# Kernel tuning notes

Hardware: AMD Instinct MI355X
Metric: run time of the kernel (lower is better)

Reference implementation:

```python
import jax, jax.numpy as jnp
import numpy as np

N_NODES = 50000
N_EDGES = 800000
C_IN = 64
HID = 3
C_OUT = 128
ATTR = 6


def setup_inputs() -> dict:
    key = jax.random.key(0)
    ks = jax.random.split(key, 16)
    inp = {
        "x": jax.random.normal(ks[0], (N_NODES, C_IN), dtype=jnp.float32),
        "edge_index0": jax.random.randint(ks[1], (2, N_EDGES), 0, N_NODES, dtype=jnp.int32).astype(jnp.int64),
        "edge_attr0": jax.random.normal(ks[2], (N_EDGES, ATTR), dtype=jnp.float32),
        "edge_index1": jax.random.randint(ks[3], (2, N_EDGES), 0, N_NODES, dtype=jnp.int32).astype(jnp.int64),
        "edge_attr1": jax.random.normal(ks[4], (N_EDGES, ATTR), dtype=jnp.float32),
        "W_in0": jax.random.normal(ks[5], (ATTR, HID * C_IN), dtype=jnp.float32) * 0.1,
        "b_in0": jax.random.normal(ks[6], (HID * C_IN,), dtype=jnp.float32) * 0.1,
        "W_out0": jax.random.normal(ks[7], (HID * C_IN, C_OUT), dtype=jnp.float32) * 0.05,
        "b_out0": jax.random.normal(ks[8], (C_OUT,), dtype=jnp.float32) * 0.05,
        "W_in1": jax.random.normal(ks[9], (ATTR, HID * C_IN), dtype=jnp.float32) * 0.1,
        "b_in1": jax.random.normal(ks[10], (HID * C_IN,), dtype=jnp.float32) * 0.1,
        "W_out1": jax.random.normal(ks[11], (HID * C_IN, C_OUT), dtype=jnp.float32) * 0.05,
        "b_out1": jax.random.normal(ks[12], (C_OUT,), dtype=jnp.float32) * 0.05,
    }
    return inp


def _spatial_graph_conv(x, edge_index, edge_attr, W_in, b_in, W_out, b_out):
    # PyG MessagePassing default flow: x_j = x[edge_index[0]] (source),
    # aggregate (add) at edge_index[1] (target).
    src, dst = edge_index[0], edge_index[1]
    n_nodes, c_in = x.shape
    x_j = x[src]                                   # [E, C]
    scaling = jax.nn.relu(edge_attr @ W_in + b_in)  # [E, 3C]
    n_edges = x_j.shape[0]
    msg = (scaling.reshape(n_edges, c_in, -1) * x_j[:, :, None]).reshape(n_edges, -1)  # [E, 3C]
    aggr = jax.ops.segment_sum(msg, dst, num_segments=n_nodes)  # [N, 3C]
    return jnp.tanh(aggr @ W_out + b_out)  # [N, C_OUT]; dropout p=0 -> identity


def reference(x, edge_index0, edge_attr0, edge_index1, edge_attr1,
              W_in0, b_in0, W_out0, b_out0, W_in1, b_in1, W_out1, b_out1):
    # aGCN_conv with use_A=2: two independent SpatialGraphConv layers, concat on feature dim.
    y0 = _spatial_graph_conv(x, edge_index0, edge_attr0, W_in0, b_in0, W_out0, b_out0)
    y1 = _spatial_graph_conv(x, edge_index1, edge_attr1, W_in1, b_in1, W_out1, b_out1)
    return jnp.concatenate([y0, y1], axis=1)  # [N, 2*C_OUT]
```

## Files before the change

kernel.cpp:

```cpp
#include <hip/hip_runtime.h>

#define N_NODES 50000
#define N_EDGES 800000
#define C_IN 64
#define HID 3
#define C_OUTC 128
#define ATTR 6
#define K3 192
#define NREAL 1563
#define NBK2 1564
#define CAP2 768
#define EPB2 2048
#define P1B2 391
#define AGS 200
#define SORTCAP (CAP2 + 96)

typedef _Float16 half8  __attribute__((ext_vector_type(8)));
typedef float    floatx4 __attribute__((ext_vector_type(4)));

#define RFL(x) __builtin_amdgcn_readfirstlane((int)(x))

static __device__ __forceinline__ float lo16f(unsigned v) {
    unsigned short s = (unsigned short)(v & 0xFFFF);
    _Float16 h;
    __builtin_memcpy(&h, &s, 2);
    return (float)h;
}
static __device__ __forceinline__ float hi16f(unsigned v) { return lo16f(v >> 16); }

static __device__ __forceinline__ unsigned pkh(float a, float b) {
    _Float16 ha = (_Float16)a, hb = (_Float16)b;
    unsigned short xa, xbits;
    __builtin_memcpy(&xa, &ha, 2);
    __builtin_memcpy(&xbits, &hb, 2);
    return (unsigned)xa | ((unsigned)xbits << 16);
}

__global__ __launch_bounds__(512)
void pass1(const int* __restrict__ ei0, const int* __restrict__ ei1,
           const float* __restrict__ ea0, const float* __restrict__ ea1,
           int* __restrict__ cursor, int4* __restrict__ seg)
{
    __shared__ int s_cnt[NBK2], s_ofs[NBK2], s_pos[NBK2], s_gbase[NBK2];
    __shared__ int4 st_es[EPB2];
    __shared__ unsigned short st_b[EPB2];
    __shared__ int wsum[8];
    const int t = threadIdx.x, lane = t & 63, wid = t >> 6;
    const int l = (blockIdx.x >= P1B2) ? 1 : 0;
    const int* ei = l ? ei1 : ei0;
    const float* __restrict__ ea = l ? ea1 : ea0;
    const int base = (blockIdx.x - l * P1B2) * EPB2;

    for (int i = t; i < NBK2; i += 512) s_cnt[i] = 0;
    __syncthreads();

    int src[4], dst[4];
    unsigned pa0[4], pa1[4], pa2[4];
    const int e0 = base + t * 4;
    if (e0 + 3 < N_EDGES) {
        const int4 s0 = *(const int4*)(ei + e0);
        const int4 d0 = *(const int4*)(ei + N_EDGES + e0);
        src[0]=s0.x; src[1]=s0.y; src[2]=s0.z; src[3]=s0.w;
        dst[0]=d0.x; dst[1]=d0.y; dst[2]=d0.z; dst[3]=d0.w;
#pragma unroll
        for (int j = 0; j < 4; ++j) {
            const float2 q01 = *(const float2*)(ea + (size_t)(e0 + j) * ATTR + 0);
            const float2 q23 = *(const float2*)(ea + (size_t)(e0 + j) * ATTR + 2);
            const float2 q45 = *(const float2*)(ea + (size_t)(e0 + j) * ATTR + 4);
            pa0[j] = pkh(q01.x, q01.y);
            pa1[j] = pkh(q23.x, q23.y);
            pa2[j] = pkh(q45.x, q45.y);
        }
    } else {
#pragma unroll
        for (int j = 0; j < 4; ++j) {
            const int e = e0 + j;
            if (e < N_EDGES) {
                src[j] = ei[e]; dst[j] = ei[N_EDGES + e];
                const float2 q01 = *(const float2*)(ea + (size_t)e * ATTR + 0);
                const float2 q23 = *(const float2*)(ea + (size_t)e * ATTR + 2);
                const float2 q45 = *(const float2*)(ea + (size_t)e * ATTR + 4);
                pa0[j] = pkh(q01.x, q01.y);
                pa1[j] = pkh(q23.x, q23.y);
                pa2[j] = pkh(q45.x, q45.y);
            } else dst[j] = -1;
        }
    }
#pragma unroll
    for (int j = 0; j < 4; ++j)
        if (dst[j] >= 0) atomicAdd(&s_cnt[dst[j] >> 5], 1);
    __syncthreads();

    int v0 = 0, v1 = 0, v2 = 0, v3 = 0;
    const bool hasq = (t < NBK2 / 4);
    if (hasq) {
        v0 = s_cnt[4 * t + 0]; v1 = s_cnt[4 * t + 1];
        v2 = s_cnt[4 * t + 2]; v3 = s_cnt[4 * t + 3];
    }
    const int pv = v0 + v1 + v2 + v3;
    int incl = pv;
#pragma unroll
    for (int off = 1; off < 64; off <<= 1) {
        const int u = __shfl_up(incl, off, 64);
        if (lane >= off) incl += u;
    }
    if (lane == 63) wsum[wid] = incl;
    __syncthreads();
    if (wid == 0) {
        int s = (lane < 8) ? wsum[lane] : 0;
#pragma unroll
        for (int off = 1; off < 8; off <<= 1) {
            const int u = __shfl_up(s, off, 64);
            if (lane >= off) s += u;
        }
        if (lane < 8) wsum[lane] = s;
    }
    __syncthreads();
    const int ex = (wid ? wsum[wid - 1] : 0) + (incl - pv);
    if (hasq) {
        s_ofs[4 * t + 0] = ex;                s_pos[4 * t + 0] = ex;
        s_ofs[4 * t + 1] = ex + v0;           s_pos[4 * t + 1] = ex + v0;
        s_ofs[4 * t + 2] = ex + v0 + v1;      s_pos[4 * t + 2] = ex + v0 + v1;
        s_ofs[4 * t + 3] = ex + v0 + v1 + v2; s_pos[4 * t + 3] = ex + v0 + v1 + v2;
    }
    __syncthreads();

    for (int i = t; i < NBK2; i += 512)
        if (s_cnt[i]) s_gbase[i] = atomicAdd(&cursor[l * NBK2 + i], s_cnt[i]);

#pragma unroll
    for (int j = 0; j < 4; ++j) {
        if (dst[j] >= 0) {
            const int b = dst[j] >> 5;
            const int p = atomicAdd(&s_pos[b], 1);
            st_es[p] = make_int4(src[j] | ((dst[j] & 31) << 16),
                                 (int)pa0[j], (int)pa1[j], (int)pa2[j]);
            st_b[p]  = (unsigned short)b;
        }
    }
    __syncthreads();

    const int total = (N_EDGES - base < EPB2) ? (N_EDGES - base) : EPB2;
    for (int j = t; j < total; j += 512) {
        const int b = st_b[j];
        const int g = s_gbase[b] + (j - s_ofs[b]);
        if (g < CAP2) seg[(size_t)(l * NREAL + b) * CAP2 + g] = st_es[j];
    }
}

#define XW4 ((N_NODES * C_IN) / 4)
#define XW4Z (((N_NODES + 1) * C_IN) / 4)
__global__ __launch_bounds__(256)
void xcvt(const float* __restrict__ x, unsigned short* __restrict__ xb)
{
    const int i = blockIdx.x * 256 + threadIdx.x;
    if (i < XW4) {
        const float4 v = ((const float4*)x)[i];
        ushort4 o;
        unsigned u;
        u = __float_as_uint(v.x); o.x = (unsigned short)((u + 0x7FFF + ((u >> 16) & 1)) >> 16);
        u = __float_as_uint(v.y); o.y = (unsigned short)((u + 0x7FFF + ((u >> 16) & 1)) >> 16);
        u = __float_as_uint(v.z); o.z = (unsigned short)((u + 0x7FFF + ((u >> 16) & 1)) >> 16);
        u = __float_as_uint(v.w); o.w = (unsigned short)((u + 0x7FFF + ((u >> 16) & 1)) >> 16);
        ((ushort4*)xb)[i] = o;
    } else if (i < XW4Z) {
        ((ushort4*)xb)[i] = make_ushort4(0, 0, 0, 0);
    }
}

__global__ __launch_bounds__(256)
void wcvt(const float* __restrict__ Wo0, const float* __restrict__ Wo1,
          _Float16* __restrict__ w16)
{
    const int i = blockIdx.x * 256 + threadIdx.x;
    if (i < 2 * K3 * C_OUTC) {
        const int layer = i / (K3 * C_OUTC), r = i % (K3 * C_OUTC);
        const int k = r / C_OUTC, n = r % C_OUTC;
        const float v = (layer ? Wo1 : Wo0)[r];
        w16[((size_t)layer * (K3 / 8) + (k >> 3)) * C_OUTC * 8 + n * 8 + (k & 7)] =
            (_Float16)v;
    }
}

#define EDGE_FMA(P0, P1, P2, HJ)                                               \
    {                                                                          \
        const float xv = __uint_as_float((unsigned)(HJ) << 16);                \
        const float A0 = lo16f(P0), A1 = hi16f(P0);                            \
        const float A2 = lo16f(P1), A3 = hi16f(P1);                            \
        const float A4 = lo16f(P2), A5 = hi16f(P2);                            \
        float s0 = bb[0], s1 = bb[1], s2 = bb[2];                              \
        s0 = fmaf(A0, w[0][0], s0); s1 = fmaf(A0, w[0][1], s1); s2 = fmaf(A0, w[0][2], s2); \
        s0 = fmaf(A1, w[1][0], s0); s1 = fmaf(A1, w[1][1], s1); s2 = fmaf(A1, w[1][2], s2); \
        s0 = fmaf(A2, w[2][0], s0); s1 = fmaf(A2, w[2][1], s1); s2 = fmaf(A2, w[2][2], s2); \
        s0 = fmaf(A3, w[3][0], s0); s1 = fmaf(A3, w[3][1], s1); s2 = fmaf(A3, w[3][2], s2); \
        s0 = fmaf(A4, w[4][0], s0); s1 = fmaf(A4, w[4][1], s1); s2 = fmaf(A4, w[4][2], s2); \
        s0 = fmaf(A5, w[5][0], s0); s1 = fmaf(A5, w[5][1], s1); s2 = fmaf(A5, w[5][2], s2); \
        acc0 = fmaf(fmaxf(s0, 0.f), xv, acc0);                                 \
        acc1 = fmaf(fmaxf(s1, 0.f), xv, acc1);                                 \
        acc2 = fmaf(fmaxf(s2, 0.f), xv, acc2);                                 \
    }

__global__ __launch_bounds__(256, 6)
void mega(const unsigned short* __restrict__ xb,
          const float* __restrict__ Wi0, const float* __restrict__ bi0,
          const float* __restrict__ bo0,
          const float* __restrict__ Wi1, const float* __restrict__ bi1,
          const float* __restrict__ bo1,
          const _Float16* __restrict__ w16,
          const int* __restrict__ cursor, const int4* __restrict__ seg,
          float* __restrict__ out)
{
    __shared__ __attribute__((aligned(16))) int4 sorted[SORTCAP];
    __shared__ __attribute__((aligned(16))) _Float16 agg[32 * AGS];
    __shared__ int hist[32], cur[32], pex[32];
    const int t = threadIdx.x, lane = t & 63, wv = t >> 6;
    const int l = (blockIdx.x >= NREAL) ? 1 : 0;
    const int bk = blockIdx.x - l * NREAL;
    const int nodebase = bk * 32;
    const float* Wi = l ? Wi1 : Wi0;
    const float* bi = l ? bi1 : bi0;
    const float* bo = l ? bo1 : bo0;

    const int col = 3 * lane;
    float w[ATTR][HID], bb[HID];
#pragma unroll
    for (int k = 0; k < ATTR; ++k)
#pragma unroll
        for (int h = 0; h < HID; ++h)
            w[k][h] = Wi[k * K3 + col + h];
#pragma unroll
    for (int h = 0; h < HID; ++h) bb[h] = bi[col + h];

    const int S0 = cursor[l * NBK2 + bk];
    const int S = (S0 < CAP2) ? S0 : CAP2;
    const int4* __restrict__ segb = seg + (size_t)(l * NREAL + bk) * CAP2;

    if (t < 32) hist[t] = 0;
    __syncthreads();

    int4 r0 = make_int4(0, 0, 0, 0), r1 = r0, r2 = r0;
    const bool h0 = (t < S), h1 = (t + 256 < S), h2 = (t + 512 < S);
    if (h0) r0 = segb[t];
    if (h1) r1 = segb[t + 256];
    if (h2) r2 = segb[t + 512];
    if (h0) atomicAdd(&hist[(r0.x >> 16) & 31], 1);
    if (h1) atomicAdd(&hist[(r1.x >> 16) & 31], 1);
    if (h2) atomicAdd(&hist[(r2.x >> 16) & 31], 1);
    __syncthreads();

    if (t < 32) {
        const int v = hist[t];
        const int pvv = (v + 3) & ~3;
        int incl = pvv;
#pragma unroll
        for (int off = 1; off < 32; off <<= 1) {
            const int u = __shfl_up(incl, off, 64);
            if (t >= off) incl += u;
        }
        cur[t] = incl - pvv;
        pex[t] = incl - pvv;
    }
    __syncthreads();

    if (h0) sorted[atomicAdd(&cur[(r0.x >> 16) & 31], 1)] = r0;
    if (h1) sorted[atomicAdd(&cur[(r1.x >> 16) & 31], 1)] = r1;
    if (h2) sorted[atomicAdd(&cur[(r2.x >> 16) & 31], 1)] = r2;
    if (t < 32) {
        const int v = hist[t], pvv = (v + 3) & ~3;
        for (int p = pex[t] + v; p < pex[t] + pvv; ++p)
            sorted[p] = make_int4(N_NODES, 0, 0, 0);
    }
    __syncthreads();

    int cx = 0, px = 0;
    if (lane < 8) { cx = hist[wv * 8 + lane]; px = pex[wv * 8 + lane]; }

#pragma unroll 1
    for (int u = 0; u < 8; ++u) {
        const int cnt = RFL(__shfl(cx, u));
        const int dl = wv * 8 + u;
        _Float16* ap = &agg[dl * AGS + col];
        if (cnt == 0) {
            ap[0] = (_Float16)0.f; ap[1] = (_Float16)0.f; ap[2] = (_Float16)0.f;
            continue;
        }
        const int base = RFL(__shfl(px, u));
        const int nch = (cnt + 3) >> 2;
        const int4* __restrict__ ep = &sorted[base];

        float acc0 = 0.f, acc1 = 0.f, acc2 = 0.f;

        int4 f0 = ep[0], f1 = ep[1], f2 = ep[2], f3 = ep[3];
        int s0_ = f0.x & 0xFFFF; unsigned p00 = f0.y, p01 = f0.z, p02 = f0.w;
        int s1_ = f1.x & 0xFFFF; unsigned p10 = f1.y, p11 = f1.z, p12 = f1.w;
        int s2_ = f2.x & 0xFFFF; unsigned p20 = f2.y, p21 = f2.z, p22 = f2.w;
        int s3_ = f3.x & 0xFFFF; unsigned p30 = f3.y, p31 = f3.z, p32 = f3.w;
        unsigned short hv0 = xb[(size_t)(unsigned)s0_ * C_IN + lane];
        unsigned short hv1 = xb[(size_t)(unsigned)s1_ * C_IN + lane];
        unsigned short hv2 = xb[(size_t)(unsigned)s2_ * C_IN + lane];
        unsigned short hv3 = xb[(size_t)(unsigned)s3_ * C_IN + lane];

#pragma unroll 1
        for (int c = 1; c < nch; ++c) {
            const int4 g0 = ep[4 * c + 0], g1 = ep[4 * c + 1];
            const int4 g2 = ep[4 * c + 2], g3 = ep[4 * c + 3];
            EDGE_FMA(p00, p01, p02, hv0);
            EDGE_FMA(p10, p11, p12, hv1);
            EDGE_FMA(p20, p21, p22, hv2);
            EDGE_FMA(p30, p31, p32, hv3);
            s0_ = g0.x & 0xFFFF; p00 = g0.y; p01 = g0.z; p02 = g0.w;
            s1_ = g1.x & 0xFFFF; p10 = g1.y; p11 = g1.z; p12 = g1.w;
            s2_ = g2.x & 0xFFFF; p20 = g2.y; p21 = g2.z; p22 = g2.w;
            s3_ = g3.x & 0xFFFF; p30 = g3.y; p31 = g3.z; p32 = g3.w;
            hv0 = xb[(size_t)(unsigned)s0_ * C_IN + lane];
            hv1 = xb[(size_t)(unsigned)s1_ * C_IN + lane];
            hv2 = xb[(size_t)(unsigned)s2_ * C_IN + lane];
            hv3 = xb[(size_t)(unsigned)s3_ * C_IN + lane];
        }
        EDGE_FMA(p00, p01, p02, hv0);
        EDGE_FMA(p10, p11, p12, hv1);
        EDGE_FMA(p20, p21, p22, hv2);
        EDGE_FMA(p30, p31, p32, hv3);

        ap[0] = (_Float16)acc0; ap[1] = (_Float16)acc1; ap[2] = (_Float16)acc2;
    }
    __syncthreads();

    const int r0r = (wv >> 1) * 16;
    const int c0 = (wv & 1) * 64;
    const int lr = lane & 15, kg = lane >> 4;
    const _Float16* __restrict__ wb = w16 + (size_t)l * (K3 / 8) * C_OUTC * 8;

    floatx4 acc[4];
#pragma unroll
    for (int nt = 0; nt < 4; ++nt) acc[nt] = (floatx4){0.f, 0.f, 0.f, 0.f};

#pragma unroll
    for (int ks = 0; ks < 6; ++ks) {
        const int kb = ks * 32;
        const half8 a = *(const half8*)(&agg[(r0r + lr) * AGS + kb + kg * 8]);
#pragma unroll
        for (int nt = 0; nt < 4; ++nt) {
            const int n = c0 + nt * 16 + lr;
            const half8 bf = *(const half8*)(wb + ((size_t)(ks * 4 + kg) * C_OUTC + n) * 8);
            acc[nt] = __builtin_amdgcn_mfma_f32_16x16x32_f16(a, bf, acc[nt], 0, 0, 0);
        }
    }

#pragma unroll
    for (int nt = 0; nt < 4; ++nt) {
        const int n = c0 + nt * 16 + lr;
        const float bv = bo[n];
#pragma unroll
        for (int r = 0; r < 4; ++r) {
            const int node = nodebase + r0r + kg * 4 + r;
            if (node < N_NODES)
                out[(size_t)node * (2 * C_OUTC) + l * C_OUTC + n] =
                    tanhf(acc[nt][r] + bv);
        }
    }
}

extern "C" void kernel_launch(void* const* d_in, const int* in_sizes, int n_in,
                              void* d_out, int out_size, void* d_ws, size_t ws_size,
                              hipStream_t stream) {
    const float* x   = (const float*)d_in[0];
    const int*   ei0 = (const int*)d_in[1];
    const float* ea0 = (const float*)d_in[2];
    const int*   ei1 = (const int*)d_in[3];
    const float* ea1 = (const float*)d_in[4];
    const float* Wi0 = (const float*)d_in[5];
    const float* bi0 = (const float*)d_in[6];
    const float* Wo0 = (const float*)d_in[7];
    const float* bo0 = (const float*)d_in[8];
    const float* Wi1 = (const float*)d_in[9];
    const float* bi1 = (const float*)d_in[10];
    const float* Wo1 = (const float*)d_in[11];
    const float* bo1 = (const float*)d_in[12];
    float* out = (float*)d_out;

    int* cursor        = (int*)d_ws;
    unsigned short* xb = (unsigned short*)(cursor + 2 * NBK2);
    int4* seg          = (int4*)(xb + (size_t)(N_NODES + 1) * C_IN);
    _Float16* w16      = (_Float16*)(seg + (size_t)2 * NREAL * CAP2);

    hipMemsetAsync(cursor, 0, 2 * NBK2 * sizeof(int), stream);
    xcvt<<<(XW4Z + 255) / 256, 256, 0, stream>>>(x, xb);
    wcvt<<<(2 * K3 * C_OUTC + 255) / 256, 256, 0, stream>>>(Wo0, Wo1, w16);
    pass1<<<2 * P1B2, 512, 0, stream>>>(ei0, ei1, ea0, ea1, cursor, seg);
    mega<<<2 * NREAL, 256, 0, stream>>>(xb,
                                        Wi0, bi0, bo0,
                                        Wi1, bi1, bo1,
                                        w16, cursor, seg, out);
}
```

Measured before the change: 276.1 us.

## Merge prep kernels and replace shared-memory bucketing with direct global atomic scatter

Folds the memset, x conversion and weight conversion into one prep kernel, cutting three launches and a memset to one. The block-local count/scan/stage pass1 is replaced by a simple per-edge kernel that takes a global atomic on the bucket cursor and writes its packed edge record straight to the segment buffer. This drops shared-memory staging and the block scans, but it sends every edge through a global atomic (about 1.6M atomics spread over ~3k counters) and gives scattered, uncoalesced int4 writes. Edge order within a bucket becomes nondeterministic, so the float summation order can vary from run to run.

```diff
diff --git a/kernel.cpp b/kernel.cpp
--- a/kernel.cpp
+++ b/kernel.cpp
@@ -10,10 +10,15 @@
 #define NREAL 1563
 #define NBK2 1564
 #define CAP2 768
-#define EPB2 2048
-#define P1B2 391
 #define AGS 200
 #define SORTCAP (CAP2 + 96)
+
+#define XW4 ((N_NODES * C_IN) / 4)
+#define XW4Z (((N_NODES + 1) * C_IN) / 4)
+#define PREP_XB ((XW4Z + 255) / 256)
+#define PREP_W  ((2 * K3 * C_OUTC + 255) / 256)
+#define PREP_C  ((2 * NBK2 + 255) / 256)
+#define SCB ((N_EDGES + 255) / 256)
 
 typedef _Float16 half8  __attribute__((ext_vector_type(8)));
 typedef float    floatx4 __attribute__((ext_vector_type(4)));
@@ -36,150 +41,65 @@
     return (unsigned)xa | ((unsigned)xbits << 16);
 }
 
-__global__ __launch_bounds__(512)
-void pass1(const int* __restrict__ ei0, const int* __restrict__ ei1,
-           const float* __restrict__ ea0, const float* __restrict__ ea1,
-           int* __restrict__ cursor, int4* __restrict__ seg)
+__global__ __launch_bounds__(256)
+void prep(const float* __restrict__ x, unsigned short* __restrict__ xb,
+          const float* __restrict__ Wo0, const float* __restrict__ Wo1,
+          _Float16* __restrict__ w16, int* __restrict__ cursor)
 {
-    __shared__ int s_cnt[NBK2], s_ofs[NBK2], s_pos[NBK2], s_gbase[NBK2];
-    __shared__ int4 st_es[EPB2];
-    __shared__ unsigned short st_b[EPB2];
-    __shared__ int wsum[8];
-    const int t = threadIdx.x, lane = t & 63, wid = t >> 6;
-    const int l = (blockIdx.x >= P1B2) ? 1 : 0;
-    const int* ei = l ? ei1 : ei0;
+    const int bid = blockIdx.x;
+    if (bid < PREP_XB) {
+        const int i = bid * 256 + threadIdx.x;
+        if (i < XW4) {
+            const float4 v = ((const float4*)x)[i];
+            ushort4 o;
+            unsigned u;
+            u = __float_as_uint(v.x); o.x = (unsigned short)((u + 0x7FFF + ((u >> 16) & 1)) >> 16);
+            u = __float_as_uint(v.y); o.y = (unsigned short)((u + 0x7FFF + ((u >> 16) & 1)) >> 16);
+            u = __float_as_uint(v.z); o.z = (unsigned short)((u + 0x7FFF + ((u >> 16) & 1)) >> 16);
+            u = __float_as_uint(v.w); o.w = (unsigned short)((u + 0x7FFF + ((u >> 16) & 1)) >> 16);
+            ((ushort4*)xb)[i] = o;
+        } else if (i < XW4Z) {
+            ((ushort4*)xb)[i] = make_ushort4(0, 0, 0, 0);
+        }
+    } else if (bid < PREP_XB + PREP_W) {
+        const int i = (bid - PREP_XB) * 256 + threadIdx.x;
+        if (i < 2 * K3 * C_OUTC) {
+            const int layer = i / (K3 * C_OUTC), r = i % (K3 * C_OUTC);
+            const int k = r / C_OUTC, n = r % C_OUTC;
+            const float v = (layer ? Wo1 : Wo0)[r];
+            w16[((size_t)layer * (K3 / 8) + (k >> 3)) * C_OUTC * 8 + n * 8 + (k & 7)] =
+                (_Float16)v;
+        }
+    } else {
+        const int i = (bid - PREP_XB - PREP_W) * 256 + threadIdx.x;
+        if (i < 2 * NBK2) cursor[i] = 0;
+    }
+}
+
+__global__ __launch_bounds__(256)
+void scat(const int* __restrict__ ei0, const int* __restrict__ ei1,
+          const float* __restrict__ ea0, const float* __restrict__ ea1,
+          int* __restrict__ cursor, int4* __restrict__ seg)
+{
+    const int bid = blockIdx.x;
+    const int l = (bid >= SCB) ? 1 : 0;
+    const int e = (bid - l * SCB) * 256 + threadIdx.x;
+    if (e >= N_EDGES) return;
+    const int* __restrict__ ei = l ? ei1 : ei0;
     const float* __restrict__ ea = l ? ea1 : ea0;
-    const int base = (blockIdx.x - l * P1B2) * EPB2;
-
-    for (int i = t; i < NBK2; i += 512) s_cnt[i] = 0;
-    __syncthreads();
-
-    int src[4], dst[4];
-    unsigned pa0[4], pa1[4], pa2[4];
-    const int e0 = base + t * 4;
-    if (e0 + 3 < N_EDGES) {
-        const int4 s0 = *(const int4*)(ei + e0);
-        const int4 d0 = *(const int4*)(ei + N_EDGES + e0);
-        src[0]=s0.x; src[1]=s0.y; src[2]=s0.z; src[3]=s0.w;
-        dst[0]=d0.x; dst[1]=d0.y; dst[2]=d0.z; dst[3]=d0.w;
-#pragma unroll
-        for (int j = 0; j < 4; ++j) {
-            const float2 q01 = *(const float2*)(ea + (size_t)(e0 + j) * ATTR + 0);
-            const float2 q23 = *(const float2*)(ea + (size_t)(e0 + j) * ATTR + 2);
-            const float2 q45 = *(const float2*)(ea + (size_t)(e0 + j) * ATTR + 4);
-            pa0[j] = pkh(q01.x, q01.y);
-            pa1[j] = pkh(q23.x, q23.y);
-            pa2[j] = pkh(q45.x, q45.y);
-        }
-    } else {
-#pragma unroll
-        for (int j = 0; j < 4; ++j) {
-            const int e = e0 + j;
-            if (e < N_EDGES) {
-                src[j] = ei[e]; dst[j] = ei[N_EDGES + e];
-                const float2 q01 = *(const float2*)(ea + (size_t)e * ATTR + 0);
-                const float2 q23 = *(const float2*)(ea + (size_t)e * ATTR + 2);
-                const float2 q45 = *(const float2*)(ea + (size_t)e * ATTR + 4);
-                pa0[j] = pkh(q01.x, q01.y);
-                pa1[j] = pkh(q23.x, q23.y);
-                pa2[j] = pkh(q45.x, q45.y);
-            } else dst[j] = -1;
-        }
-    }
-#pragma unroll
-    for (int j = 0; j < 4; ++j)
-        if (dst[j] >= 0) atomicAdd(&s_cnt[dst[j] >> 5], 1);
-    __syncthreads();
-
-    int v0 = 0, v1 = 0, v2 = 0, v3 = 0;
-    const bool hasq = (t < NBK2 / 4);
-    if (hasq) {
-        v0 = s_cnt[4 * t + 0]; v1 = s_cnt[4 * t + 1];
-        v2 = s_cnt[4 * t + 2]; v3 = s_cnt[4 * t + 3];
-    }
-    const int pv = v0 + v1 + v2 + v3;
-    int incl = pv;
-#pragma unroll
-    for (int off = 1; off < 64; off <<= 1) {
-        const int u = __shfl_up(incl, off, 64);
-        if (lane >= off) incl += u;
-    }
-    if (lane == 63) wsum[wid] = incl;
-    __syncthreads();
-    if (wid == 0) {
-        int s = (lane < 8) ? wsum[lane] : 0;
-#pragma unroll
-        for (int off = 1; off < 8; off <<= 1) {
-            const int u = __shfl_up(s, off, 64);
-            if (lane >= off) s += u;
-        }
-        if (lane < 8) wsum[lane] = s;
-    }
-    __syncthreads();
-    const int ex = (wid ? wsum[wid - 1] : 0) + (incl - pv);
-    if (hasq) {
-        s_ofs[4 * t + 0] = ex;                s_pos[4 * t + 0] = ex;
-        s_ofs[4 * t + 1] = ex + v0;           s_pos[4 * t + 1] = ex + v0;
-        s_ofs[4 * t + 2] = ex + v0 + v1;      s_pos[4 * t + 2] = ex + v0 + v1;
-        s_ofs[4 * t + 3] = ex + v0 + v1 + v2; s_pos[4 * t + 3] = ex + v0 + v1 + v2;
-    }
-    __syncthreads();
-
-    for (int i = t; i < NBK2; i += 512)
-        if (s_cnt[i]) s_gbase[i] = atomicAdd(&cursor[l * NBK2 + i], s_cnt[i]);
-
-#pragma unroll
-    for (int j = 0; j < 4; ++j) {
-        if (dst[j] >= 0) {
-            const int b = dst[j] >> 5;
-            const int p = atomicAdd(&s_pos[b], 1);
-            st_es[p] = make_int4(src[j] | ((dst[j] & 31) << 16),
-                                 (int)pa0[j], (int)pa1[j], (int)pa2[j]);
-            st_b[p]  = (unsigned short)b;
-        }
-    }
-    __syncthreads();
-
-    const int total = (N_EDGES - base < EPB2) ? (N_EDGES - base) : EPB2;
-    for (int j = t; j < total; j += 512) {
-        const int b = st_b[j];
-        const int g = s_gbase[b] + (j - s_ofs[b]);
-        if (g < CAP2) seg[(size_t)(l * NREAL + b) * CAP2 + g] = st_es[j];
-    }
-}
-
-#define XW4 ((N_NODES * C_IN) / 4)
-#define XW4Z (((N_NODES + 1) * C_IN) / 4)
-__global__ __launch_bounds__(256)
-void xcvt(const float* __restrict__ x, unsigned short* __restrict__ xb)
-{
-    const int i = blockIdx.x * 256 + threadIdx.x;
-    if (i < XW4) {
-        const float4 v = ((const float4*)x)[i];
-        ushort4 o;
-        unsigned u;
-        u = __float_as_uint(v.x); o.x = (unsigned short)((u + 0x7FFF + ((u >> 16) & 1)) >> 16);
-        u = __float_as_uint(v.y); o.y = (unsigned short)((u + 0x7FFF + ((u >> 16) & 1)) >> 16);
-        u = __float_as_uint(v.z); o.z = (unsigned short)((u + 0x7FFF + ((u >> 16) & 1)) >> 16);
-        u = __float_as_uint(v.w); o.w = (unsigned short)((u + 0x7FFF + ((u >> 16) & 1)) >> 16);
-        ((ushort4*)xb)[i] = o;
-    } else if (i < XW4Z) {
-        ((ushort4*)xb)[i] = make_ushort4(0, 0, 0, 0);
-    }
-}
-
-__global__ __launch_bounds__(256)
-void wcvt(const float* __restrict__ Wo0, const float* __restrict__ Wo1,
-          _Float16* __restrict__ w16)
-{
-    const int i = blockIdx.x * 256 + threadIdx.x;
-    if (i < 2 * K3 * C_OUTC) {
-        const int layer = i / (K3 * C_OUTC), r = i % (K3 * C_OUTC);
-        const int k = r / C_OUTC, n = r % C_OUTC;
-        const float v = (layer ? Wo1 : Wo0)[r];
-        w16[((size_t)layer * (K3 / 8) + (k >> 3)) * C_OUTC * 8 + n * 8 + (k & 7)] =
-            (_Float16)v;
-    }
+
+    const int src = ei[e], dst = ei[N_EDGES + e];
+    const float2 q01 = *(const float2*)(ea + (size_t)e * ATTR + 0);
+    const float2 q23 = *(const float2*)(ea + (size_t)e * ATTR + 2);
+    const float2 q45 = *(const float2*)(ea + (size_t)e * ATTR + 4);
+
+    const int b = dst >> 5;
+    const int pos = atomicAdd(&cursor[l * NBK2 + b], 1);
+    if (pos < CAP2)
+        seg[(size_t)(l * NREAL + b) * CAP2 + pos] =
+            make_int4(src | ((dst & 31) << 16),
+                      (int)pkh(q01.x, q01.y), (int)pkh(q23.x, q23.y),
+                      (int)pkh(q45.x, q45.y));
 }
 
 #define EDGE_FMA(P0, P1, P2, HJ)                                               \
@@ -384,10 +304,8 @@
     int4* seg          = (int4*)(xb + (size_t)(N_NODES + 1) * C_IN);
     _Float16* w16      = (_Float16*)(seg + (size_t)2 * NREAL * CAP2);
 
-    hipMemsetAsync(cursor, 0, 2 * NBK2 * sizeof(int), stream);
-    xcvt<<<(XW4Z + 255) / 256, 256, 0, stream>>>(x, xb);
-    wcvt<<<(2 * K3 * C_OUTC + 255) / 256, 256, 0, stream>>>(Wo0, Wo1, w16);
-    pass1<<<2 * P1B2, 512, 0, stream>>>(ei0, ei1, ea0, ea1, cursor, seg);
+    prep<<<PREP_XB + PREP_W + PREP_C, 256, 0, stream>>>(x, xb, Wo0, Wo1, w16, cursor);
+    scat<<<2 * SCB, 256, 0, stream>>>(ei0, ei1, ea0, ea1, cursor, seg);
     mega<<<2 * NREAL, 256, 0, stream>>>(xb,
                                         Wi0, bi0, bo0,
                                         Wi1, bi1, bo1,
```

New measurement: 465.2 us. +68.5%, slower.
